# Performance work log

Measured on AMD Instinct MI355X. Metric: run time of the kernel, lower is better.

## Reference

```python
import jax, jax.numpy as jnp
import numpy as np

INNER_DIM = 64
NEG = 1e12


def _rotate_half_interleaved(x):
    # stack([-x[..., 1::2], x[..., ::2]], -1).reshape(x.shape)
    x2 = jnp.stack([-x[..., 1::2], x[..., ::2]], axis=-1)
    return x2.reshape(x.shape)


def setup_inputs() -> dict:
    key = jax.random.key(0)
    k1, k2 = jax.random.split(key)
    B, S, H = 16, 512, 768
    T, D = 9, INNER_DIM
    hidden = jax.random.normal(k1, (B, S, H), dtype=jnp.float32)
    W = jax.random.normal(k2, (H, T * 2 * D), dtype=jnp.float32) * 0.02
    b = jnp.zeros((T * 2 * D,), dtype=jnp.float32)
    attention_mask = jnp.ones((B, S), dtype=jnp.int32)
    return {"hidden": hidden, "W": W, "b": b, "attention_mask": attention_mask}


def reference(hidden, W, b, attention_mask):
    B, S, H = hidden.shape
    D = INNER_DIM
    T = W.shape[1] // (2 * D)

    # dense + split into per-type q/k: [B, S, T, 2D]
    out = (jnp.einsum('bsh,hc->bsc', hidden, W) + b).reshape(B, S, T, 2 * D)
    qw, kw = out[..., :D], out[..., D:]

    # inline sinusoidal RoPE (interleaved sin/cos layout)
    pos = jnp.arange(S, dtype=jnp.float32)[:, None]            # [S, 1]
    inv = jnp.power(10000.0, -2.0 * jnp.arange(D // 2, dtype=jnp.float32) / D)
    ang = pos * inv                                            # [S, D/2]
    cos_pos = jnp.repeat(jnp.cos(ang), 2, axis=-1)[None, :, None, :]  # [1,S,1,D]
    sin_pos = jnp.repeat(jnp.sin(ang), 2, axis=-1)[None, :, None, :]
    qw = qw * cos_pos + _rotate_half_interleaved(qw) * sin_pos
    kw = kw * cos_pos + _rotate_half_interleaved(kw) * sin_pos

    # pairwise scores per entity type: [B, T, S, S]
    logits = jnp.einsum('bmtd,bntd->btmn', qw, kw)

    # padding mask (key dim only, as in original expand) with large negative
    pm = attention_mask.astype(logits.dtype)[:, None, None, :]  # [B,1,1,S]
    logits = logits * pm - (1.0 - pm) * NEG

    # strict lower-triangular mask (only upper-triangular spans valid)
    tril = jnp.tril(jnp.ones((S, S), dtype=logits.dtype), -1)
    logits = logits - tril * NEG

    return logits / np.sqrt(D).astype(np.float32)
```

## Files before the change

kernel.cpp:

```cpp
#include <hip/hip_runtime.h>
#include <cstdint>
#include <cstddef>

#define NEG_C 1000000000000.0f

typedef __bf16 bf16x8 __attribute__((ext_vector_type(8)));
typedef float f32x4 __attribute__((ext_vector_type(4)));

union Frag {
    int4 i;
    bf16x8 b;
};

__device__ __forceinline__ unsigned short f32_to_bf16_rne(float f) {
    unsigned int u = __float_as_uint(f);
    u += 0x7fffu + ((u >> 16) & 1u);
    return (unsigned short)(u >> 16);
}
__device__ __forceinline__ float bf16u_to_f32(unsigned short h) {
    return __uint_as_float(((unsigned int)h) << 16);
}

__global__ void convert_hidden_kernel(const float* __restrict__ src,
                                      unsigned short* __restrict__ dst, int n4) {
    int idx = blockIdx.x * blockDim.x + threadIdx.x;
    if (idx >= n4) return;
    float4 v = ((const float4*)src)[idx];
    ushort4 o;
    o.x = f32_to_bf16_rne(v.x);
    o.y = f32_to_bf16_rne(v.y);
    o.z = f32_to_bf16_rne(v.z);
    o.w = f32_to_bf16_rne(v.w);
    ((ushort4*)dst)[idx] = o;
}

__global__ void transpose_w_kernel(const float* __restrict__ W,
                                   unsigned short* __restrict__ WT) {
    __shared__ unsigned short tile[32][33];
    int bx = blockIdx.x;
    int by = blockIdx.y;
    int x = threadIdx.x & 31;
    int y0 = threadIdx.x >> 5;
#pragma unroll
    for (int yy = 0; yy < 32; yy += 8) {
        int k = by * 32 + y0 + yy;
        int n = bx * 32 + x;
        tile[y0 + yy][x] = f32_to_bf16_rne(W[(size_t)k * 1152 + n]);
    }
    __syncthreads();
#pragma unroll
    for (int yy = 0; yy < 32; yy += 8) {
        int n = bx * 32 + y0 + yy;
        int k = by * 32 + x;
        WT[(size_t)n * 768 + k] = tile[x][y0 + yy];
    }
}

__global__ __launch_bounds__(256, 2) void gemm1_kernel(
    const unsigned short* __restrict__ Ah, const unsigned short* __restrict__ WT,
    const float* __restrict__ bias, unsigned short* __restrict__ proj) {
    const int K = 768, N = 1152;
    __shared__ unsigned short As[128 * 32];
    __shared__ unsigned short Bs[128 * 32];
    int tid = threadIdx.x;
    int lane = tid & 63;
    int wave = tid >> 6;
    int bm = blockIdx.x * 128;
    int bn = blockIdx.y * 128;
    int wm = (wave & 1) * 64;
    int wn = (wave >> 1) * 64;
    int col_l = lane & 15;
    int kg = (lane >> 4) * 8;

    f32x4 acc[4][4] = {};

    for (int k0 = 0; k0 < K; k0 += 32) {
        __syncthreads();
#pragma unroll
        for (int p = 0; p < 2; ++p) {
            int c = p * 256 + tid;
            int row = c >> 2;
            int ko = (c & 3) * 8;
            *(int4*)(As + row * 32 + ko) =
                *(const int4*)(Ah + (size_t)(bm + row) * K + k0 + ko);
            *(int4*)(Bs + row * 32 + ko) =
                *(const int4*)(WT + (size_t)(bn + row) * K + k0 + ko);
        }
        __syncthreads();
        Frag a[4], bfr[4];
#pragma unroll
        for (int i = 0; i < 4; ++i) {
            a[i].i   = *(const int4*)(As + (wm + i * 16 + col_l) * 32 + kg);
            bfr[i].i = *(const int4*)(Bs + (wn + i * 16 + col_l) * 32 + kg);
        }
#pragma unroll
        for (int i = 0; i < 4; ++i)
#pragma unroll
            for (int j = 0; j < 4; ++j)
                acc[i][j] = __builtin_amdgcn_mfma_f32_16x16x32_bf16(
                    a[i].b, bfr[j].b, acc[i][j], 0, 0, 0);
    }
    int row_q = (lane >> 4) * 4;
#pragma unroll
    for (int i = 0; i < 4; ++i) {
#pragma unroll
        for (int j = 0; j < 4; ++j) {
            int gn = bn + wn + j * 16 + col_l;
            float bb = bias[gn];
#pragma unroll
            for (int r = 0; r < 4; ++r) {
                int gm = bm + wm + i * 16 + row_q + r;
                proj[(size_t)gm * N + gn] = f32_to_bf16_rne(acc[i][j][r] + bb);
            }
        }
    }
}

__global__ void rope_kernel(unsigned short* __restrict__ proj) {
    int idx = blockIdx.x * blockDim.x + threadIdx.x;
    int i = idx & 31;
    int rest = idx >> 5;
    int t = rest % 9;
    int rest2 = rest / 9;
    int s = rest2 & 511;
    int b = rest2 >> 9;
    float inv = exp2f(-0.41524101186091903f * (float)i);
    float ang = (float)s * inv;
    float sn, cs;
    sincosf(ang, &sn, &cs);
    unsigned int* p = (unsigned int*)(proj + (((size_t)(b * 512 + s) * 9) + t) * 128);
    unsigned int q = p[i];
    float q0 = bf16u_to_f32((unsigned short)(q & 0xffffu));
    float q1 = bf16u_to_f32((unsigned short)(q >> 16));
    float r0 = q0 * cs - q1 * sn;
    float r1 = q1 * cs + q0 * sn;
    p[i] = (unsigned int)f32_to_bf16_rne(r0) | ((unsigned int)f32_to_bf16_rne(r1) << 16);
    unsigned int k = p[32 + i];
    float k0 = bf16u_to_f32((unsigned short)(k & 0xffffu));
    float k1 = bf16u_to_f32((unsigned short)(k >> 16));
    float t0 = k0 * cs - k1 * sn;
    float t1 = k1 * cs + k0 * sn;
    p[32 + i] = (unsigned int)f32_to_bf16_rne(t0) | ((unsigned int)f32_to_bf16_rne(t1) << 16);
}

__global__ __launch_bounds__(256, 2) void gemm2_kernel(
    const unsigned short* __restrict__ proj, const int* __restrict__ mask,
    float* __restrict__ out) {
    __shared__ unsigned short Qs[128 * 64];
    __shared__ unsigned short Ks[128 * 64];
    int bid = blockIdx.x;
    int batch = bid >> 4;
    int tl = bid & 15;
    int tm = tl >> 2, tn = tl & 3;
    int b = batch / 9, t = batch - b * 9;
    int tid = threadIdx.x, lane = tid & 63, wave = tid >> 6;
    int wm = (wave & 1) * 64, wn = (wave >> 1) * 64;
    int col_l = lane & 15;
    size_t out_base = ((size_t)b * 9 + t) * 512 * 512;

    if (tm > tn) {
#pragma unroll 4
        for (int r = 0; r < 128; r += 8) {
            int row = r + (tid >> 5);
            int c4 = (tid & 31) * 4;
            int gm = tm * 128 + row;
            int gn = tn * 128 + c4;
            float4 v;
            float* po = out + out_base + (size_t)gm * 512 + gn;
#pragma unroll
            for (int q = 0; q < 4; ++q) {
                float pm = (float)mask[b * 512 + gn + q];
                ((float*)&v)[q] = (-(1.0f - pm) * NEG_C - NEG_C) * 0.125f;
            }
            *(float4*)po = v;
        }
        return;
    }

#pragma unroll
    for (int p = 0; p < 4; ++p) {
        int c = p * 256 + tid;
        int row = c >> 3;
        int ko = (c & 7) * 8;
        *(int4*)(Qs + row * 64 + ko) = *(const int4*)(
            proj + (((size_t)(b * 512 + tm * 128 + row) * 9) + t) * 128 + ko);
        *(int4*)(Ks + row * 64 + ko) = *(const int4*)(
            proj + (((size_t)(b * 512 + tn * 128 + row) * 9) + t) * 128 + 64 + ko);
    }
    __syncthreads();

    f32x4 acc[4][4] = {};
#pragma unroll
    for (int ks = 0; ks < 2; ++ks) {
        Frag a[4], bfr[4];
        int kg = ks * 32 + (lane >> 4) * 8;
#pragma unroll
        for (int i = 0; i < 4; ++i) {
            a[i].i   = *(const int4*)(Qs + (wm + i * 16 + col_l) * 64 + kg);
            bfr[i].i = *(const int4*)(Ks + (wn + i * 16 + col_l) * 64 + kg);
        }
#pragma unroll
        for (int i = 0; i < 4; ++i)
#pragma unroll
            for (int j = 0; j < 4; ++j)
                acc[i][j] = __builtin_amdgcn_mfma_f32_16x16x32_bf16(
                    a[i].b, bfr[j].b, acc[i][j], 0, 0, 0);
    }

    int row_q = (lane >> 4) * 4;
#pragma unroll
    for (int i = 0; i < 4; ++i) {
#pragma unroll
        for (int j = 0; j < 4; ++j) {
            int gn = tn * 128 + wn + j * 16 + col_l;
            float pm = (float)mask[b * 512 + gn];
#pragma unroll
            for (int r = 0; r < 4; ++r) {
                int gm = tm * 128 + wm + i * 16 + row_q + r;
                float v = acc[i][j][r] * pm - (1.0f - pm) * NEG_C;
                if (gm > gn) v -= NEG_C;
                out[out_base + (size_t)gm * 512 + gn] = v * 0.125f;
            }
        }
    }
}

extern "C" void kernel_launch(void* const* d_in, const int* in_sizes, int n_in,
                              void* d_out, int out_size, void* d_ws, size_t ws_size,
                              hipStream_t stream) {
    const float* hidden = (const float*)d_in[0];
    const float* W      = (const float*)d_in[1];
    const float* bias   = (const float*)d_in[2];
    const int*   mask   = (const int*)d_in[3];
    float* out = (float*)d_out;

    char* ws = (char*)d_ws;
    unsigned short* Ah   = (unsigned short*)(ws);
    unsigned short* WT   = (unsigned short*)(ws + 12582912);
    unsigned short* proj = (unsigned short*)(ws + 14352384);

    convert_hidden_kernel<<<6144, 256, 0, stream>>>(hidden, Ah, 1572864);
    dim3 gt(36, 24);
    transpose_w_kernel<<<gt, 256, 0, stream>>>(W, WT);
    dim3 g1(64, 9);
    gemm1_kernel<<<g1, 256, 0, stream>>>(Ah, WT, bias, proj);
    rope_kernel<<<9216, 256, 0, stream>>>(proj);
    gemm2_kernel<<<2304, 256, 0, stream>>>(proj, mask, out);
}
```

Before: 235.6 us.

## Fuse RoPE into GEMM1 epilogue and use async swizzled LDS loads

Removes the separate RoPE kernel by applying the rotation in the GEMM1 epilogue. The adjacent interleaved pair value comes from a lane shuffle, and the sine and cosine are computed per output element. It also switches the GEMM1 and GEMM2 tile loads to direct global-to-LDS async copies with an XOR swizzle to avoid bank conflicts, and doubles the GEMM1 K-step to 64. This saves the RoPE kernel's read-modify-write pass over proj, but does more sincos work in the epilogue and rounds to bf16 only once, after rotation.

```diff
diff --git a/kernel.cpp b/kernel.cpp
--- a/kernel.cpp
+++ b/kernel.cpp
@@ -17,8 +17,12 @@
     u += 0x7fffu + ((u >> 16) & 1u);
     return (unsigned short)(u >> 16);
 }
-__device__ __forceinline__ float bf16u_to_f32(unsigned short h) {
-    return __uint_as_float(((unsigned int)h) << 16);
+
+__device__ __forceinline__ void async_copy16(const void* g, void* l) {
+    __builtin_amdgcn_global_load_lds(
+        (const __attribute__((address_space(1))) unsigned int*)(uintptr_t)g,
+        (__attribute__((address_space(3))) unsigned int*)(uintptr_t)l,
+        16, 0, 0);
 }
 
 __global__ void convert_hidden_kernel(const float* __restrict__ src,
@@ -60,8 +64,8 @@
     const unsigned short* __restrict__ Ah, const unsigned short* __restrict__ WT,
     const float* __restrict__ bias, unsigned short* __restrict__ proj) {
     const int K = 768, N = 1152;
-    __shared__ unsigned short As[128 * 32];
-    __shared__ unsigned short Bs[128 * 32];
+    __shared__ unsigned short As[128 * 64];
+    __shared__ unsigned short Bs[128 * 64];
     int tid = threadIdx.x;
     int lane = tid & 63;
     int wave = tid >> 6;
@@ -70,77 +74,70 @@
     int wm = (wave & 1) * 64;
     int wn = (wave >> 1) * 64;
     int col_l = lane & 15;
-    int kg = (lane >> 4) * 8;
-
+    int qg = lane >> 4;
+
+    int c0 = wave * 4 * 64 + lane;
     f32x4 acc[4][4] = {};
 
-    for (int k0 = 0; k0 < K; k0 += 32) {
+    for (int k0 = 0; k0 < K; k0 += 64) {
         __syncthreads();
 #pragma unroll
-        for (int p = 0; p < 2; ++p) {
-            int c = p * 256 + tid;
-            int row = c >> 2;
-            int ko = (c & 3) * 8;
-            *(int4*)(As + row * 32 + ko) =
-                *(const int4*)(Ah + (size_t)(bm + row) * K + k0 + ko);
-            *(int4*)(Bs + row * 32 + ko) =
-                *(const int4*)(WT + (size_t)(bn + row) * K + k0 + ko);
+        for (int q = 0; q < 4; ++q) {
+            int c = c0 + q * 64;
+            int r = c >> 3;
+            int g = (c & 7) ^ (r & 7);
+            async_copy16(Ah + (size_t)(bm + r) * K + k0 + g * 8,
+                         As + (size_t)(wave * 4 + q) * 512);
+            async_copy16(WT + (size_t)(bn + r) * K + k0 + g * 8,
+                         Bs + (size_t)(wave * 4 + q) * 512);
         }
         __syncthreads();
-        Frag a[4], bfr[4];
+        Frag a[2][4], bfr[2][4];
+#pragma unroll
+        for (int ks = 0; ks < 2; ++ks) {
+            int g = ks * 4 + qg;
+#pragma unroll
+            for (int i = 0; i < 4; ++i) {
+                int ra = wm + i * 16 + col_l;
+                int rb = wn + i * 16 + col_l;
+                a[ks][i].i   = *(const int4*)(As + ra * 64 + ((g ^ (ra & 7)) * 8));
+                bfr[ks][i].i = *(const int4*)(Bs + rb * 64 + ((g ^ (rb & 7)) * 8));
+            }
+        }
+#pragma unroll
+        for (int ks = 0; ks < 2; ++ks)
+#pragma unroll
+            for (int i = 0; i < 4; ++i)
+#pragma unroll
+                for (int j = 0; j < 4; ++j)
+                    acc[i][j] = __builtin_amdgcn_mfma_f32_16x16x32_bf16(
+                        a[ks][i].b, bfr[ks][j].b, acc[i][j], 0, 0, 0);
+    }
+
+    int row_q = qg * 4;
+#pragma unroll
+    for (int j = 0; j < 4; ++j) {
+        int cn = wn + j * 16 + col_l;
+        int gn = bn + cn;
+        int pair = (cn >> 1) & 31;
+        int odd = cn & 1;
+        float inv = exp2f(-0.41524101186091903f * (float)pair);
+        float bb = bias[gn];
 #pragma unroll
         for (int i = 0; i < 4; ++i) {
-            a[i].i   = *(const int4*)(As + (wm + i * 16 + col_l) * 32 + kg);
-            bfr[i].i = *(const int4*)(Bs + (wn + i * 16 + col_l) * 32 + kg);
-        }
-#pragma unroll
-        for (int i = 0; i < 4; ++i)
-#pragma unroll
-            for (int j = 0; j < 4; ++j)
-                acc[i][j] = __builtin_amdgcn_mfma_f32_16x16x32_bf16(
-                    a[i].b, bfr[j].b, acc[i][j], 0, 0, 0);
-    }
-    int row_q = (lane >> 4) * 4;
-#pragma unroll
-    for (int i = 0; i < 4; ++i) {
-#pragma unroll
-        for (int j = 0; j < 4; ++j) {
-            int gn = bn + wn + j * 16 + col_l;
-            float bb = bias[gn];
 #pragma unroll
             for (int r = 0; r < 4; ++r) {
                 int gm = bm + wm + i * 16 + row_q + r;
-                proj[(size_t)gm * N + gn] = f32_to_bf16_rne(acc[i][j][r] + bb);
-            }
-        }
-    }
-}
-
-__global__ void rope_kernel(unsigned short* __restrict__ proj) {
-    int idx = blockIdx.x * blockDim.x + threadIdx.x;
-    int i = idx & 31;
-    int rest = idx >> 5;
-    int t = rest % 9;
-    int rest2 = rest / 9;
-    int s = rest2 & 511;
-    int b = rest2 >> 9;
-    float inv = exp2f(-0.41524101186091903f * (float)i);
-    float ang = (float)s * inv;
-    float sn, cs;
-    sincosf(ang, &sn, &cs);
-    unsigned int* p = (unsigned int*)(proj + (((size_t)(b * 512 + s) * 9) + t) * 128);
-    unsigned int q = p[i];
-    float q0 = bf16u_to_f32((unsigned short)(q & 0xffffu));
-    float q1 = bf16u_to_f32((unsigned short)(q >> 16));
-    float r0 = q0 * cs - q1 * sn;
-    float r1 = q1 * cs + q0 * sn;
-    p[i] = (unsigned int)f32_to_bf16_rne(r0) | ((unsigned int)f32_to_bf16_rne(r1) << 16);
-    unsigned int k = p[32 + i];
-    float k0 = bf16u_to_f32((unsigned short)(k & 0xffffu));
-    float k1 = bf16u_to_f32((unsigned short)(k >> 16));
-    float t0 = k0 * cs - k1 * sn;
-    float t1 = k1 * cs + k0 * sn;
-    p[32 + i] = (unsigned int)f32_to_bf16_rne(t0) | ((unsigned int)f32_to_bf16_rne(t1) << 16);
+                float v = acc[i][j][r] + bb;
+                float p = __shfl_xor(v, 1, 64);
+                float ang = (float)(gm & 511) * inv;
+                float sn, cs;
+                sincosf(ang, &sn, &cs);
+                float o = odd ? (v * cs + p * sn) : (v * cs - p * sn);
+                proj[(size_t)gm * N + gn] = f32_to_bf16_rne(o);
+            }
+        }
+    }
 }
 
 __global__ __launch_bounds__(256, 2) void gemm2_kernel(
@@ -156,6 +153,7 @@
     int tid = threadIdx.x, lane = tid & 63, wave = tid >> 6;
     int wm = (wave & 1) * 64, wn = (wave >> 1) * 64;
     int col_l = lane & 15;
+    int qg = lane >> 4;
     size_t out_base = ((size_t)b * 9 + t) * 512 * 512;
 
     if (tm > tn) {
@@ -166,26 +164,27 @@
             int gm = tm * 128 + row;
             int gn = tn * 128 + c4;
             float4 v;
-            float* po = out + out_base + (size_t)gm * 512 + gn;
 #pragma unroll
             for (int q = 0; q < 4; ++q) {
                 float pm = (float)mask[b * 512 + gn + q];
                 ((float*)&v)[q] = (-(1.0f - pm) * NEG_C - NEG_C) * 0.125f;
             }
-            *(float4*)po = v;
+            *(float4*)(out + out_base + (size_t)gm * 512 + gn) = v;
         }
         return;
     }
 
-#pragma unroll
-    for (int p = 0; p < 4; ++p) {
-        int c = p * 256 + tid;
-        int row = c >> 3;
-        int ko = (c & 7) * 8;
-        *(int4*)(Qs + row * 64 + ko) = *(const int4*)(
-            proj + (((size_t)(b * 512 + tm * 128 + row) * 9) + t) * 128 + ko);
-        *(int4*)(Ks + row * 64 + ko) = *(const int4*)(
-            proj + (((size_t)(b * 512 + tn * 128 + row) * 9) + t) * 128 + 64 + ko);
+    const unsigned short* qbase = proj + (((size_t)(b * 512 + tm * 128) * 9) + t) * 128;
+    const unsigned short* kbase = proj + (((size_t)(b * 512 + tn * 128) * 9) + t) * 128 + 64;
+#pragma unroll
+    for (int q = 0; q < 4; ++q) {
+        int c = (wave * 4 + q) * 64 + lane;
+        int r = c >> 3;
+        int g = (c & 7) ^ (r & 7);
+        async_copy16(qbase + (size_t)r * 1152 + g * 8,
+                     Qs + (size_t)(wave * 4 + q) * 512);
+        async_copy16(kbase + (size_t)r * 1152 + g * 8,
+                     Ks + (size_t)(wave * 4 + q) * 512);
     }
     __syncthreads();
 
@@ -193,11 +192,13 @@
 #pragma unroll
     for (int ks = 0; ks < 2; ++ks) {
         Frag a[4], bfr[4];
-        int kg = ks * 32 + (lane >> 4) * 8;
+        int g = ks * 4 + qg;
 #pragma unroll
         for (int i = 0; i < 4; ++i) {
-            a[i].i   = *(const int4*)(Qs + (wm + i * 16 + col_l) * 64 + kg);
-            bfr[i].i = *(const int4*)(Ks + (wn + i * 16 + col_l) * 64 + kg);
+            int ra = wm + i * 16 + col_l;
+            int rb = wn + i * 16 + col_l;
+            a[i].i   = *(const int4*)(Qs + ra * 64 + ((g ^ (ra & 7)) * 8));
+            bfr[i].i = *(const int4*)(Ks + rb * 64 + ((g ^ (rb & 7)) * 8));
         }
 #pragma unroll
         for (int i = 0; i < 4; ++i)
@@ -207,7 +208,7 @@
                     a[i].b, bfr[j].b, acc[i][j], 0, 0, 0);
     }
 
-    int row_q = (lane >> 4) * 4;
+    int row_q = qg * 4;
 #pragma unroll
     for (int i = 0; i < 4; ++i) {
 #pragma unroll
@@ -244,6 +245,5 @@
     transpose_w_kernel<<<gt, 256, 0, stream>>>(W, WT);
     dim3 g1(64, 9);
     gemm1_kernel<<<g1, 256, 0, stream>>>(Ah, WT, bias, proj);
-    rope_kernel<<<9216, 256, 0, stream>>>(proj);
     gemm2_kernel<<<2304, 256, 0, stream>>>(proj, mask, out);
 }
```

After: 376.5 us. 1.6x slower.
